# Optimization experiments

Measured on AMD Instinct MI355X. Metric: run time of the kernel, lower is better.

Reference implementation:

```python
import jax, jax.numpy as jnp
import numpy as np

N = 100000
E = 3200000
D_IN = 256
D_OUT = 128
ALPHA = 0.2  # tf.nn.leaky_relu default slope


def setup_inputs() -> dict:
    key = jax.random.key(0)
    ks = jax.random.split(key, 8)
    feat = jax.random.normal(ks[0], (N, D_IN), dtype=jnp.float32)
    row = jax.random.randint(ks[1], (E,), 0, N, dtype=jnp.int32)
    col = jax.random.randint(ks[2], (E,), 0, N, dtype=jnp.int32)
    # Dense(out_dim, use_bias=False)
    W = jax.random.normal(ks[3], (D_IN, D_OUT), dtype=jnp.float32) / np.sqrt(D_IN)
    # attn_l / attn_r: Dense(1) with bias
    al_w = jax.random.normal(ks[4], (D_OUT, 1), dtype=jnp.float32) / np.sqrt(D_OUT)
    al_b = jnp.zeros((1,), dtype=jnp.float32)
    ar_w = jax.random.normal(ks[5], (D_OUT, 1), dtype=jnp.float32) / np.sqrt(D_OUT)
    ar_b = jnp.zeros((1,), dtype=jnp.float32)
    bias = jnp.zeros((D_OUT,), dtype=jnp.float32)
    return {"feat": feat, "row": row, "col": col, "W": W,
            "al_w": al_w, "al_b": al_b, "ar_w": ar_w, "ar_b": ar_b, "bias": bias}


def reference(feat, row, col, W, al_w, al_b, ar_w, ar_b, bias):
    # seq_fts = W(feat)  [N, D_OUT]
    seq_fts = feat @ W
    # per-node attention scalars  [N]
    f1 = (seq_fts @ al_w + al_b)[:, 0]
    f2 = (seq_fts @ ar_w + ar_b)[:, 0]
    # per-edge logits (gather) + leaky_relu  [E]
    logits = jax.nn.leaky_relu(f1[row] + f2[col], negative_slope=ALPHA)
    # sparse (segment) softmax over each destination row
    m = jax.ops.segment_max(logits, row, num_segments=N)   # [N], -inf for empty rows (unused)
    e = jnp.exp(logits - m[row])                            # [E]
    s = jax.ops.segment_sum(e, row, num_segments=N)         # [N]
    coefs = e / s[row]                                      # [E]
    # spmm: vals[i] = sum_{e: row[e]=i} coefs[e] * seq_fts[col[e]]
    vals = jax.ops.segment_sum(coefs[:, None] * seq_fts[col], row, num_segments=N)
    return vals + bias  # act is None
```

## Files before the change

kernel.cpp:

```cpp
#include <hip/hip_runtime.h>
#include <math.h>

#define N_NODES 100000
#define N_EDGES 3200000
#define D_IN    256
#define D_OUT   128
#define ALPHA   0.2f

#define NB_HIST 125
#define CHUNK   (N_EDGES / NB_HIST)
#define HWORDS  (N_NODES / 4)
#define NGRP    5
#define GLEN    (NB_HIST / NGRP)

typedef short bf8_t  __attribute__((ext_vector_type(8)));
typedef float f4_t   __attribute__((ext_vector_type(4)));

__device__ __forceinline__ unsigned int f2bf(float x) {
    unsigned int u = __float_as_uint(x);
    return (u + 0x7fffu + ((u >> 16) & 1u)) >> 16;
}
__device__ __forceinline__ unsigned int packbf(float lo, float hi) {
    return f2bf(lo) | (f2bf(hi) << 16);
}
__device__ __forceinline__ float bflo(unsigned int v) { return __uint_as_float(v << 16); }
__device__ __forceinline__ float bfhi(unsigned int v) { return __uint_as_float(v & 0xffff0000u); }

__global__ void wt_kernel(const float* __restrict__ W, short* __restrict__ WTs) {
    int o = blockIdx.x * 256 + threadIdx.x;
    int j    = o & 7;
    int lane = (o >> 3) & 63;
    int nt   = (o >> 9) & 7;
    int kc   = o >> 12;
    int n = nt * 16 + (lane & 15);
    int k = kc * 32 + (lane >> 4) * 8 + j;
    WTs[o] = (short)f2bf(W[k * 128 + n]);
}

__global__ __launch_bounds__(256) void gemm_kernel(const float* __restrict__ feat,
                                                   const short* __restrict__ WTs,
                                                   const float* __restrict__ al_w,
                                                   const float* __restrict__ al_b,
                                                   const float* __restrict__ ar_w,
                                                   const float* __restrict__ ar_b,
                                                   unsigned int* __restrict__ seqb,
                                                   float* __restrict__ f1,
                                                   float* __restrict__ f2) {
    __shared__ char ldsA[64 * 528];
    const int tid = threadIdx.x;
    const int tb  = blockIdx.x * 64;

#pragma unroll
    for (int i = 0; i < 16; i++) {
        int idx = i * 256 + tid;
        int r   = idx >> 6;
        int c4  = idx & 63;
        int gr  = tb + r; if (gr >= N_NODES) gr = N_NODES - 1;
        float4 v = ((const float4*)feat)[(size_t)gr * 64 + c4];
        *(uint2*)(ldsA + r * 528 + c4 * 8) =
            make_uint2(packbf(v.x, v.y), packbf(v.z, v.w));
    }
    __syncthreads();

    const int w    = tid >> 6;
    const int lane = tid & 63;
    const int m    = lane & 15;
    const int q    = lane >> 4;

    const char*  aptr = ldsA + (w * 16 + m) * 528 + q * 16;
    const short* bb   = WTs + (size_t)lane * 8;

    f4_t acc[8];
#pragma unroll
    for (int nt = 0; nt < 8; nt++) acc[nt] = (f4_t)(0.f);

#pragma unroll
    for (int kc = 0; kc < 8; kc++) {
        bf8_t a = *(const bf8_t*)(aptr + kc * 64);
#pragma unroll
        for (int nt = 0; nt < 8; nt++) {
            bf8_t b = *(const bf8_t*)(bb + (kc * 8 + nt) * 512);
            acc[nt] = __builtin_amdgcn_mfma_f32_16x16x32_bf16(a, b, acc[nt], 0, 0, 0);
        }
    }

    const int node_base = tb + w * 16 + q * 4;
#pragma unroll
    for (int nt = 0; nt < 8; nt++) {
#pragma unroll
        for (int j = 0; j < 4; j++) {
            float own   = acc[nt][j];
            float other = __shfl_xor(own, 1);
            int node = node_base + j;
            if (!(lane & 1) && node < N_NODES)
                seqb[(size_t)node * 64 + nt * 8 + (m >> 1)] = packbf(own, other);
        }
    }

    float p1[4] = {0.f, 0.f, 0.f, 0.f}, p2[4] = {0.f, 0.f, 0.f, 0.f};
#pragma unroll
    for (int nt = 0; nt < 8; nt++) {
        float av = al_w[nt * 16 + m];
        float rv = ar_w[nt * 16 + m];
#pragma unroll
        for (int j = 0; j < 4; j++) {
            p1[j] += acc[nt][j] * av;
            p2[j] += acc[nt][j] * rv;
        }
    }
#pragma unroll
    for (int j = 0; j < 4; j++) {
#pragma unroll
        for (int mk = 1; mk < 16; mk <<= 1) {
            p1[j] += __shfl_xor(p1[j], mk);
            p2[j] += __shfl_xor(p2[j], mk);
        }
    }
    if (m == 0) {
        float alb = al_b[0], arb = ar_b[0];
#pragma unroll
        for (int j = 0; j < 4; j++) {
            int node = node_base + j;
            if (node < N_NODES) {
                f1[node] = p1[j] + alb;
                f2[node] = p2[j] + arb;
            }
        }
    }
}

__global__ __launch_bounds__(1024) void hist_kernel(const int* __restrict__ row,
                                                    unsigned char* __restrict__ localrank,
                                                    unsigned int* __restrict__ histpk) {
    __shared__ unsigned int h[HWORDS];
    const int tid = threadIdx.x;
    for (int i = tid; i < HWORDS; i += 1024) h[i] = 0u;
    __syncthreads();

    const int base = blockIdx.x * CHUNK;
#pragma unroll
    for (int it = 0; it < CHUNK / 1024; it++) {
        int e = base + it * 1024 + tid;
        int r = row[e];
        unsigned int sh  = (unsigned int)(r & 3) * 8u;
        unsigned int old = atomicAdd(&h[r >> 2], 1u << sh);
        localrank[e] = (unsigned char)((old >> sh) & 0xffu);
    }
    __syncthreads();

    unsigned int* dst = histpk + (size_t)blockIdx.x * HWORDS;
    for (int i = tid; i < HWORDS; i += 1024) dst[i] = h[i];
}

__global__ __launch_bounds__(256) void scanbA_kernel(const unsigned int* __restrict__ histpk,
                                                     unsigned int* __restrict__ blockpre,
                                                     unsigned int* __restrict__ gsum) {
    int id = blockIdx.x * 256 + threadIdx.x;
    if (id >= NGRP * HWORDS) return;
    int g = id / HWORDS;
    int w = id - g * HWORDS;
    const unsigned int* hp = histpk   + (size_t)(g * GLEN) * HWORDS + w;
    unsigned int*       bp = blockpre + (size_t)(g * GLEN) * HWORDS + w;
    unsigned int run = 0u;
#pragma unroll 5
    for (int i = 0; i < GLEN; i++) {
        unsigned int hv = hp[(size_t)i * HWORDS];
        bp[(size_t)i * HWORDS] = run;
        run += hv;
    }
    gsum[(size_t)g * HWORDS + w] = run;
}

__global__ __launch_bounds__(256) void scanbB_kernel(unsigned int* __restrict__ gsum,
                                                     uint4* __restrict__ cnt4) {
    int w = blockIdx.x * 256 + threadIdx.x;
    if (w >= HWORDS) return;
    unsigned int run = 0u;
#pragma unroll
    for (int g = 0; g < NGRP; g++) {
        unsigned int v = gsum[(size_t)g * HWORDS + w];
        gsum[(size_t)g * HWORDS + w] = run;
        run += v;
    }
    cnt4[w] = make_uint4(run & 0xffu, (run >> 8) & 0xffu,
                         (run >> 16) & 0xffu, run >> 24);
}

__global__ void scan1(const unsigned int* __restrict__ cnt,
                      unsigned int* __restrict__ offs,
                      unsigned int* __restrict__ bsums) {
    __shared__ unsigned int s[256];
    int t = threadIdx.x;
    int i = blockIdx.x * 256 + t;
    unsigned int v = (i < N_NODES) ? cnt[i] : 0u;
    s[t] = v; __syncthreads();
    for (int d = 1; d < 256; d <<= 1) {
        unsigned int x = (t >= d) ? s[t - d] : 0u;
        __syncthreads();
        s[t] += x;
        __syncthreads();
    }
    if (i < N_NODES) offs[i] = s[t] - v;
    if (t == 255) bsums[blockIdx.x] = s[255];
}

__global__ void scan2(const unsigned int* __restrict__ bsums,
                      unsigned int* __restrict__ bexcl, int nb) {
    __shared__ unsigned int s[512];
    int t = threadIdx.x;
    unsigned int v = (t < nb) ? bsums[t] : 0u;
    s[t] = v; __syncthreads();
    for (int d = 1; d < 512; d <<= 1) {
        unsigned int x = (t >= d) ? s[t - d] : 0u;
        __syncthreads();
        s[t] += x;
        __syncthreads();
    }
    if (t < nb) bexcl[t] = s[t] - v;
}

__global__ void scan3(unsigned int* __restrict__ offs,
                      const unsigned int* __restrict__ bexcl) {
    int i = blockIdx.x * 256 + threadIdx.x;
    if (i < N_NODES) offs[i] += bexcl[blockIdx.x];
}

__global__ __launch_bounds__(256) void offsg_kernel(const unsigned int* __restrict__ offs,
                                                    const unsigned int* __restrict__ gsum,
                                                    unsigned int* __restrict__ offs_g) {
    int id = blockIdx.x * 256 + threadIdx.x;
    if (id >= NGRP * HWORDS) return;
    int g = id / HWORDS;
    int w = id - g * HWORDS;
    unsigned int gb = gsum[(size_t)g * HWORDS + w];
    uint4 o4 = *(const uint4*)(offs + w * 4);
    uint4 r;
    r.x = o4.x + (gb & 0xffu);
    r.y = o4.y + ((gb >> 8) & 0xffu);
    r.z = o4.z + ((gb >> 16) & 0xffu);
    r.w = o4.w + (gb >> 24);
    ((uint4*)(offs_g + (size_t)g * N_NODES))[w] = r;
}

__global__ __launch_bounds__(512) void scatter_kernel(const int* __restrict__ row,
                                                      const int* __restrict__ col,
                                                      const unsigned char* __restrict__ localrank,
                                                      const unsigned int* __restrict__ blockpre,
                                                      const unsigned int* __restrict__ offs_g,
                                                      int* __restrict__ sorted_c) {
    __shared__ unsigned int wpre[HWORDS];
    const int b    = blockIdx.x >> 1;
    const int half = blockIdx.x & 1;
    const int tid  = threadIdx.x;

    const unsigned int* src = blockpre + (size_t)b * HWORDS;
    for (int i = tid; i < HWORDS; i += 512) wpre[i] = src[i];
    __syncthreads();

    const unsigned int* og = offs_g + (size_t)(b / GLEN) * N_NODES;
    const int base = b * CHUNK + half * (CHUNK / 2);
#pragma unroll 5
    for (int it = 0; it < (CHUNK / 2) / 512; it++) {
        int e = base + it * 512 + tid;
        int r = row[e];
        unsigned int bp = (wpre[r >> 2] >> ((unsigned int)(r & 3) * 8u)) & 0xffu;
        unsigned int p  = og[r] + bp + (unsigned int)localrank[e];
        __builtin_nontemporal_store(col[e], &sorted_c[p]);
    }
}

__global__ __launch_bounds__(256) void row_kernel(const uint4* __restrict__ seqb4,
                                                  const int* __restrict__ sorted_c,
                                                  const unsigned int* __restrict__ offs,
                                                  const unsigned int* __restrict__ cnt,
                                                  const float* __restrict__ f1,
                                                  const float* __restrict__ f2,
                                                  const float* __restrict__ bias,
                                                  float* __restrict__ out) {
    int wid  = (blockIdx.x * 256 + threadIdx.x) >> 6;
    int lane = threadIdx.x & 63;
    int g    = lane >> 4;
    int j4   = lane & 15;
    if (wid >= N_NODES) return;
    unsigned int start = offs[wid];
    unsigned int deg   = cnt[wid];
    const int* sc = sorted_c + start;
    float f1r = f1[wid];

    float a0 = 0.f, a1 = 0.f, a2 = 0.f, a3 = 0.f;
    float a4 = 0.f, a5 = 0.f, a6 = 0.f, a7 = 0.f, ss = 0.f;

    unsigned int k = 0;
    for (; k + 16 <= deg; k += 16) {
        int c0 = sc[k + g];
        int c1 = sc[k + 4 + g];
        int c2 = sc[k + 8 + g];
        int c3 = sc[k + 12 + g];
        uint4 v0 = seqb4[(unsigned)c0 * 16u + j4];
        uint4 v1 = seqb4[(unsigned)c1 * 16u + j4];
        uint4 v2 = seqb4[(unsigned)c2 * 16u + j4];
        uint4 v3 = seqb4[(unsigned)c3 * 16u + j4];
        float t0 = f1r + f2[c0], t1 = f1r + f2[c1];
        float t2 = f1r + f2[c2], t3 = f1r + f2[c3];
        float w0 = __expf(fmaxf(t0, ALPHA * t0));
        float w1 = __expf(fmaxf(t1, ALPHA * t1));
        float w2 = __expf(fmaxf(t2, ALPHA * t2));
        float w3 = __expf(fmaxf(t3, ALPHA * t3));
        ss += (w0 + w1) + (w2 + w3);
        a0 += w0 * bflo(v0.x); a1 += w0 * bfhi(v0.x);
        a2 += w0 * bflo(v0.y); a3 += w0 * bfhi(v0.y);
        a4 += w0 * bflo(v0.z); a5 += w0 * bfhi(v0.z);
        a6 += w0 * bflo(v0.w); a7 += w0 * bfhi(v0.w);
        a0 += w1 * bflo(v1.x); a1 += w1 * bfhi(v1.x);
        a2 += w1 * bflo(v1.y); a3 += w1 * bfhi(v1.y);
        a4 += w1 * bflo(v1.z); a5 += w1 * bfhi(v1.z);
        a6 += w1 * bflo(v1.w); a7 += w1 * bfhi(v1.w);
        a0 += w2 * bflo(v2.x); a1 += w2 * bfhi(v2.x);
        a2 += w2 * bflo(v2.y); a3 += w2 * bfhi(v2.y);
        a4 += w2 * bflo(v2.z); a5 += w2 * bfhi(v2.z);
        a6 += w2 * bflo(v2.w); a7 += w2 * bfhi(v2.w);
        a0 += w3 * bflo(v3.x); a1 += w3 * bfhi(v3.x);
        a2 += w3 * bflo(v3.y); a3 += w3 * bfhi(v3.y);
        a4 += w3 * bflo(v3.z); a5 += w3 * bfhi(v3.z);
        a6 += w3 * bflo(v3.w); a7 += w3 * bfhi(v3.w);
    }
    for (; k + 8 <= deg; k += 8) {
        int ca = sc[k + g];
        int cb = sc[k + 4 + g];
        uint4 va = seqb4[(unsigned)ca * 16u + j4];
        uint4 vb = seqb4[(unsigned)cb * 16u + j4];
        float ta = f1r + f2[ca];
        float tb = f1r + f2[cb];
        float wa = __expf(fmaxf(ta, ALPHA * ta));
        float wb = __expf(fmaxf(tb, ALPHA * tb));
        ss += wa + wb;
        a0 += wa * bflo(va.x); a1 += wa * bfhi(va.x);
        a2 += wa * bflo(va.y); a3 += wa * bfhi(va.y);
        a4 += wa * bflo(va.z); a5 += wa * bfhi(va.z);
        a6 += wa * bflo(va.w); a7 += wa * bfhi(va.w);
        a0 += wb * bflo(vb.x); a1 += wb * bfhi(vb.x);
        a2 += wb * bflo(vb.y); a3 += wb * bfhi(vb.y);
        a4 += wb * bflo(vb.z); a5 += wb * bfhi(vb.z);
        a6 += wb * bflo(vb.w); a7 += wb * bfhi(vb.w);
    }
    for (; k < deg; k += 4) {
        unsigned int ke = k + g;
        int c = sc[ke < deg ? ke : deg - 1];
        uint4 v = seqb4[(unsigned)c * 16u + j4];
        float t = f1r + f2[c];
        float w = __expf(fmaxf(t, ALPHA * t));
        if (ke >= deg) w = 0.f;
        ss += w;
        a0 += w * bflo(v.x); a1 += w * bfhi(v.x);
        a2 += w * bflo(v.y); a3 += w * bfhi(v.y);
        a4 += w * bflo(v.z); a5 += w * bfhi(v.z);
        a6 += w * bflo(v.w); a7 += w * bfhi(v.w);
    }

    a0 += __shfl_xor(a0, 16); a0 += __shfl_xor(a0, 32);
    a1 += __shfl_xor(a1, 16); a1 += __shfl_xor(a1, 32);
    a2 += __shfl_xor(a2, 16); a2 += __shfl_xor(a2, 32);
    a3 += __shfl_xor(a3, 16); a3 += __shfl_xor(a3, 32);
    a4 += __shfl_xor(a4, 16); a4 += __shfl_xor(a4, 32);
    a5 += __shfl_xor(a5, 16); a5 += __shfl_xor(a5, 32);
    a6 += __shfl_xor(a6, 16); a6 += __shfl_xor(a6, 32);
    a7 += __shfl_xor(a7, 16); a7 += __shfl_xor(a7, 32);
    ss += __shfl_xor(ss, 16); ss += __shfl_xor(ss, 32);

    if (g == 0) {
        float inv = (deg > 0) ? 1.f / ss : 0.f;
        float4 b0 = ((const float4*)bias)[j4 * 2];
        float4 b1 = ((const float4*)bias)[j4 * 2 + 1];
        float4* orow = (float4*)(out + (size_t)wid * D_OUT);
        orow[j4 * 2]     = make_float4(a0 * inv + b0.x, a1 * inv + b0.y,
                                       a2 * inv + b0.z, a3 * inv + b0.w);
        orow[j4 * 2 + 1] = make_float4(a4 * inv + b1.x, a5 * inv + b1.y,
                                       a6 * inv + b1.z, a7 * inv + b1.w);
    }
}

extern "C" void kernel_launch(void* const* d_in, const int* in_sizes, int n_in,
                              void* d_out, int out_size, void* d_ws, size_t ws_size,
                              hipStream_t stream) {
    const float* feat = (const float*)d_in[0];
    const int*   row  = (const int*)d_in[1];
    const int*   col  = (const int*)d_in[2];
    const float* W    = (const float*)d_in[3];
    const float* al_w = (const float*)d_in[4];
    const float* al_b = (const float*)d_in[5];
    const float* ar_w = (const float*)d_in[6];
    const float* ar_b = (const float*)d_in[7];
    const float* bias = (const float*)d_in[8];
    float* out = (float*)d_out;

    char* ws = (char*)d_ws;
    size_t off = 0;
    auto carve = [&](size_t bytes) -> void* {
        off = (off + 255) & ~(size_t)255;
        void* p = ws + off;
        off += bytes;
        return p;
    };
    unsigned int* seqb     = (unsigned int*)carve((size_t)N_NODES * 64 * 4);
    float*        f1       = (float*)       carve((size_t)N_NODES * 4);
    float*        f2       = (float*)       carve((size_t)N_NODES * 4);
    unsigned int* cnt      = (unsigned int*)carve((size_t)N_NODES * 4);
    unsigned int* offs     = (unsigned int*)carve((size_t)N_NODES * 4);
    unsigned int* bsums    = (unsigned int*)carve(1024 * 4);
    unsigned int* bexcl    = (unsigned int*)carve(1024 * 4);
    short*        WTs      = (short*)       carve((size_t)D_IN * D_OUT * 2);
    unsigned char* localrank = (unsigned char*)carve((size_t)N_EDGES);
    unsigned int* blockpre = (unsigned int*)carve((size_t)NB_HIST * HWORDS * 4);
    unsigned int* gsum     = (unsigned int*)carve((size_t)NGRP * HWORDS * 4);
    unsigned int* offs_g   = (unsigned int*)carve((size_t)NGRP * N_NODES * 4);
    int*          sorted_c = (int*)         carve((size_t)N_EDGES * 4);
    unsigned int* histpk   = (unsigned int*)sorted_c;
    (void)ws_size; (void)in_sizes; (void)n_in; (void)out_size;

    const int nb_nodes = (N_NODES + 255) / 256;
    const int nb_gemm  = (N_NODES + 63) / 64;
    const int nb_gw    = (NGRP * HWORDS + 255) / 256;
    const int nb_row   = N_NODES / 4;

    wt_kernel<<<(D_IN * D_OUT) / 256, 256, 0, stream>>>(W, WTs);
    gemm_kernel<<<nb_gemm, 256, 0, stream>>>(feat, WTs, al_w, al_b, ar_w, ar_b, seqb, f1, f2);
    hist_kernel<<<NB_HIST, 1024, 0, stream>>>(row, localrank, histpk);
    scanbA_kernel<<<nb_gw, 256, 0, stream>>>(histpk, blockpre, gsum);
    scanbB_kernel<<<(HWORDS + 255) / 256, 256, 0, stream>>>(gsum, (uint4*)cnt);
    scan1<<<nb_nodes, 256, 0, stream>>>(cnt, offs, bsums);
    scan2<<<1, 512, 0, stream>>>(bsums, bexcl, nb_nodes);
    scan3<<<nb_nodes, 256, 0, stream>>>(offs, bexcl);
    offsg_kernel<<<nb_gw, 256, 0, stream>>>(offs, gsum, offs_g);
    scatter_kernel<<<NB_HIST * 2, 512, 0, stream>>>(row, col, localrank,
                                                    blockpre, offs_g, sorted_c);
    row_kernel<<<nb_row, 256, 0, stream>>>((const uint4*)seqb, sorted_c, offs, cnt, f1, f2, bias, out);
}
```

Before: 450.9 us.

## Fuse degree scan kernels, merge offset fixup with group offsets, split row kernel

Merges scanbB and scan1 into one degree-scan kernel in which each thread handles four packed node counts, so the block scan covers 1024 nodes. It also folds scan3 and offsg into a single kernel that applies the block prefix and writes the per-group offsets. Together these remove two kernel launches and one round trip of the offset arrays through memory. It also replaces the nontemporal store in scatter with a plain store and splits the row aggregation kernel into two half launches, which adds a launch with no clear benefit.

```diff
diff --git a/kernel.cpp b/kernel.cpp
--- a/kernel.cpp
+++ b/kernel.cpp
@@ -171,36 +171,41 @@
     gsum[(size_t)g * HWORDS + w] = run;
 }
 
-__global__ __launch_bounds__(256) void scanbB_kernel(unsigned int* __restrict__ gsum,
-                                                     uint4* __restrict__ cnt4) {
-    int w = blockIdx.x * 256 + threadIdx.x;
-    if (w >= HWORDS) return;
-    unsigned int run = 0u;
-#pragma unroll
-    for (int g = 0; g < NGRP; g++) {
-        unsigned int v = gsum[(size_t)g * HWORDS + w];
-        gsum[(size_t)g * HWORDS + w] = run;
-        run += v;
-    }
-    cnt4[w] = make_uint4(run & 0xffu, (run >> 8) & 0xffu,
-                         (run >> 16) & 0xffu, run >> 24);
-}
-
-__global__ void scan1(const unsigned int* __restrict__ cnt,
-                      unsigned int* __restrict__ offs,
-                      unsigned int* __restrict__ bsums) {
+__global__ __launch_bounds__(256) void degscan_kernel(unsigned int* __restrict__ gsum,
+                                                      uint4* __restrict__ cnt4,
+                                                      unsigned int* __restrict__ offs,
+                                                      unsigned int* __restrict__ bsums) {
     __shared__ unsigned int s[256];
-    int t = threadIdx.x;
-    int i = blockIdx.x * 256 + t;
-    unsigned int v = (i < N_NODES) ? cnt[i] : 0u;
-    s[t] = v; __syncthreads();
+    const int t = threadIdx.x;
+    const int w = blockIdx.x * 256 + t;
+    unsigned int run = 0u, T = 0u;
+    unsigned int d0 = 0, d1 = 0, d2 = 0;
+    if (w < HWORDS) {
+#pragma unroll
+        for (int g = 0; g < NGRP; g++) {
+            unsigned int v = gsum[(size_t)g * HWORDS + w];
+            gsum[(size_t)g * HWORDS + w] = run;
+            run += v;
+        }
+        cnt4[w] = make_uint4(run & 0xffu, (run >> 8) & 0xffu,
+                             (run >> 16) & 0xffu, run >> 24);
+        d0 = run & 0xffu; d1 = (run >> 8) & 0xffu; d2 = (run >> 16) & 0xffu;
+        T = d0 + d1 + d2 + (run >> 24);
+    }
+    s[t] = T; __syncthreads();
     for (int d = 1; d < 256; d <<= 1) {
         unsigned int x = (t >= d) ? s[t - d] : 0u;
         __syncthreads();
         s[t] += x;
         __syncthreads();
     }
-    if (i < N_NODES) offs[i] = s[t] - v;
+    if (w < HWORDS) {
+        unsigned int excl = s[t] - T;
+        offs[w * 4 + 0] = excl;
+        offs[w * 4 + 1] = excl + d0;
+        offs[w * 4 + 2] = excl + d0 + d1;
+        offs[w * 4 + 3] = excl + d0 + d1 + d2;
+    }
     if (t == 255) bsums[blockIdx.x] = s[255];
 }
 
@@ -219,27 +224,20 @@
     if (t < nb) bexcl[t] = s[t] - v;
 }
 
-__global__ void scan3(unsigned int* __restrict__ offs,
-                      const unsigned int* __restrict__ bexcl) {
+__global__ __launch_bounds__(256) void scan3g_kernel(unsigned int* __restrict__ offs,
+                                                     const unsigned int* __restrict__ bexcl,
+                                                     const unsigned int* __restrict__ gsum,
+                                                     unsigned int* __restrict__ offs_g) {
     int i = blockIdx.x * 256 + threadIdx.x;
-    if (i < N_NODES) offs[i] += bexcl[blockIdx.x];
-}
-
-__global__ __launch_bounds__(256) void offsg_kernel(const unsigned int* __restrict__ offs,
-                                                    const unsigned int* __restrict__ gsum,
-                                                    unsigned int* __restrict__ offs_g) {
-    int id = blockIdx.x * 256 + threadIdx.x;
-    if (id >= NGRP * HWORDS) return;
-    int g = id / HWORDS;
-    int w = id - g * HWORDS;
-    unsigned int gb = gsum[(size_t)g * HWORDS + w];
-    uint4 o4 = *(const uint4*)(offs + w * 4);
-    uint4 r;
-    r.x = o4.x + (gb & 0xffu);
-    r.y = o4.y + ((gb >> 8) & 0xffu);
-    r.z = o4.z + ((gb >> 16) & 0xffu);
-    r.w = o4.w + (gb >> 24);
-    ((uint4*)(offs_g + (size_t)g * N_NODES))[w] = r;
+    if (i >= N_NODES) return;
+    unsigned int o = offs[i] + bexcl[i >> 10];
+    offs[i] = o;
+    unsigned int sh = (unsigned int)(i & 3) * 8u;
+#pragma unroll
+    for (int g = 0; g < NGRP; g++) {
+        unsigned int gb = (gsum[(size_t)g * HWORDS + (i >> 2)] >> sh) & 0xffu;
+        offs_g[(size_t)g * N_NODES + i] = o + gb;
+    }
 }
 
 __global__ __launch_bounds__(512) void scatter_kernel(const int* __restrict__ row,
@@ -265,23 +263,23 @@
         int r = row[e];
         unsigned int bp = (wpre[r >> 2] >> ((unsigned int)(r & 3) * 8u)) & 0xffu;
         unsigned int p  = og[r] + bp + (unsigned int)localrank[e];
-        __builtin_nontemporal_store(col[e], &sorted_c[p]);
-    }
-}
-
-__global__ __launch_bounds__(256) void row_kernel(const uint4* __restrict__ seqb4,
-                                                  const int* __restrict__ sorted_c,
-                                                  const unsigned int* __restrict__ offs,
-                                                  const unsigned int* __restrict__ cnt,
-                                                  const float* __restrict__ f1,
-                                                  const float* __restrict__ f2,
-                                                  const float* __restrict__ bias,
-                                                  float* __restrict__ out) {
-    int wid  = (blockIdx.x * 256 + threadIdx.x) >> 6;
+        sorted_c[p] = col[e];
+    }
+}
+
+__device__ __forceinline__ void row_body(int wid_base,
+                                         const uint4* __restrict__ seqb4,
+                                         const int* __restrict__ sorted_c,
+                                         const unsigned int* __restrict__ offs,
+                                         const unsigned int* __restrict__ cnt,
+                                         const float* __restrict__ f1,
+                                         const float* __restrict__ f2,
+                                         const float* __restrict__ bias,
+                                         float* __restrict__ out) {
+    int wid  = wid_base + ((blockIdx.x * 256 + threadIdx.x) >> 6);
     int lane = threadIdx.x & 63;
     int g    = lane >> 4;
     int j4   = lane & 15;
-    if (wid >= N_NODES) return;
     unsigned int start = offs[wid];
     unsigned int deg   = cnt[wid];
     const int* sc = sorted_c + start;
@@ -379,6 +377,27 @@
     }
 }
 
+__global__ __launch_bounds__(256) void rowA_kernel(const uint4* __restrict__ seqb4,
+                                                   const int* __restrict__ sorted_c,
+                                                   const unsigned int* __restrict__ offs,
+                                                   const unsigned int* __restrict__ cnt,
+                                                   const float* __restrict__ f1,
+                                                   const float* __restrict__ f2,
+                                                   const float* __restrict__ bias,
+                                                   float* __restrict__ out) {
+    row_body(0, seqb4, sorted_c, offs, cnt, f1, f2, bias, out);
+}
+__global__ __launch_bounds__(256) void rowB_kernel(const uint4* __restrict__ seqb4,
+                                                   const int* __restrict__ sorted_c,
+                                                   const unsigned int* __restrict__ offs,
+                                                   const unsigned int* __restrict__ cnt,
+                                                   const float* __restrict__ f1,
+                                                   const float* __restrict__ f2,
+                                                   const float* __restrict__ bias,
+                                                   float* __restrict__ out) {
+    row_body(N_NODES / 2, seqb4, sorted_c, offs, cnt, f1, f2, bias, out);
+}
+
 extern "C" void kernel_launch(void* const* d_in, const int* in_sizes, int n_in,
                               void* d_out, int out_size, void* d_ws, size_t ws_size,
                               hipStream_t stream) {
@@ -420,18 +439,18 @@
     const int nb_nodes = (N_NODES + 255) / 256;
     const int nb_gemm  = (N_NODES + 63) / 64;
     const int nb_gw    = (NGRP * HWORDS + 255) / 256;
-    const int nb_row   = N_NODES / 4;
+    const int nb_deg   = (HWORDS + 255) / 256;
+    const int nb_rowh  = (N_NODES / 2) / 4;
 
     wt_kernel<<<(D_IN * D_OUT) / 256, 256, 0, stream>>>(W, WTs);
     gemm_kernel<<<nb_gemm, 256, 0, stream>>>(feat, WTs, al_w, al_b, ar_w, ar_b, seqb, f1, f2);
     hist_kernel<<<NB_HIST, 1024, 0, stream>>>(row, localrank, histpk);
     scanbA_kernel<<<nb_gw, 256, 0, stream>>>(histpk, blockpre, gsum);
-    scanbB_kernel<<<(HWORDS + 255) / 256, 256, 0, stream>>>(gsum, (uint4*)cnt);
-    scan1<<<nb_nodes, 256, 0, stream>>>(cnt, offs, bsums);
-    scan2<<<1, 512, 0, stream>>>(bsums, bexcl, nb_nodes);
-    scan3<<<nb_nodes, 256, 0, stream>>>(offs, bexcl);
-    offsg_kernel<<<nb_gw, 256, 0, stream>>>(offs, gsum, offs_g);
+    degscan_kernel<<<nb_deg, 256, 0, stream>>>(gsum, (uint4*)cnt, offs, bsums);
+    scan2<<<1, 512, 0, stream>>>(bsums, bexcl, nb_deg);
+    scan3g_kernel<<<nb_nodes, 256, 0, stream>>>(offs, bexcl, gsum, offs_g);
     scatter_kernel<<<NB_HIST * 2, 512, 0, stream>>>(row, col, localrank,
                                                     blockpre, offs_g, sorted_c);
-    row_kernel<<<nb_row, 256, 0, stream>>>((const uint4*)seqb, sorted_c, offs, cnt, f1, f2, bias, out);
-}
+    rowA_kernel<<<nb_rowh, 256, 0, stream>>>((const uint4*)seqb, sorted_c, offs, cnt, f1, f2, bias, out);
+    rowB_kernel<<<nb_rowh, 256, 0, stream>>>((const uint4*)seqb, sorted_c, offs, cnt, f1, f2, bias, out);
+}
```

Result: no change. 446.7 us (-0.9%).
